# Kernel optimization log

Hardware: AMD Instinct MI355X
Metric: run time of the kernel (lower is better)

## Reference

```python
import jax, jax.numpy as jnp
import numpy as np

N_NODES = 50000


def _add_self_loops(edge_index, n):
    loop = jnp.arange(n, dtype=edge_index.dtype)
    src = jnp.concatenate([edge_index[0], loop])
    dst = jnp.concatenate([edge_index[1], loop])
    return src, dst


def _gcn_norm(src, dst, n):
    # symmetric normalization with unit edge weights (edge_weight=None)
    w = jnp.ones(src.shape[0], dtype=jnp.float32)
    deg = jax.ops.segment_sum(w, dst, num_segments=n)  # [N]
    dinv = jnp.where(deg > 0, jax.lax.rsqrt(jnp.maximum(deg, 1.0)), 0.0)
    return dinv[src] * w * dinv[dst]  # [E+N]


def _gcn_conv(x, src, dst, norm, W, b, n):
    h = x @ W                                   # [N, out] transform first (PyG order)
    msg = h[src] * norm[:, None]                # [E+N, out] gather + scale
    agg = jax.ops.segment_sum(msg, dst, num_segments=n)  # scatter-add
    return agg + b


def setup_inputs() -> dict:
    key = jax.random.key(0)
    k1, k2, k3, k4 = jax.random.split(key, 4)
    N, E, IN, HID, OUT = N_NODES, 1600000, 512, 64, 7
    x = jax.random.normal(k1, (N, IN), dtype=jnp.float32)
    edge_index = jax.random.randint(k2, (2, E), 0, N, dtype=jnp.int64)
    W1 = jax.random.normal(k3, (IN, HID), dtype=jnp.float32) * (1.0 / np.sqrt(IN))
    b1 = jnp.zeros((HID,), dtype=jnp.float32)
    W2 = jax.random.normal(k4, (HID, OUT), dtype=jnp.float32) * (1.0 / np.sqrt(HID))
    b2 = jnp.zeros((OUT,), dtype=jnp.float32)
    return {"x": x, "edge_index": edge_index, "W1": W1, "b1": b1, "W2": W2, "b2": b2}


def reference(x, edge_index, W1, b1, W2, b2):
    n = x.shape[0]
    src, dst = _add_self_loops(edge_index, n)
    norm = _gcn_norm(src, dst, n)  # graph-only, shared across layers
    h = _gcn_conv(x, src, dst, norm, W1, b1, n)
    h = jax.nn.relu(h)
    # dropout is identity in eval/inference mode
    out = _gcn_conv(h, src, dst, norm, W2, b2, n)
    return out
```

## Files before the change

kernel.cpp:

```cpp
#include <hip/hip_runtime.h>

#define N_NODES 50000
#define N_EDGES 1600000
#define DIM_IN  512
#define DIM_HID 64
#define DIM_OUT 7
#define NBUCK   196
#define PART_BLOCKS 256

using u16 = unsigned short;
using bf16x8 = __attribute__((ext_vector_type(8))) __bf16;
using f32x4  = __attribute__((ext_vector_type(4))) float;

__device__ __forceinline__ float bf2f(u16 u) {
    union { float f; unsigned int i; } v;
    v.i = ((unsigned int)u) << 16;
    return v.f;
}

__device__ __forceinline__ u16 f2bf(float f) {
    union { float f; unsigned int i; } v;
    v.f = f;
    unsigned int r = 0x7FFFu + ((v.i >> 16) & 1u);
    return (u16)((v.i + r) >> 16);
}

__global__ void k_detect(const u16* __restrict__ xw, const int* __restrict__ ei32,
                         int* __restrict__ flags) {
    __shared__ int s1[256];
    __shared__ int s2[256];
    int t = threadIdx.x;
    u16 w = xw[2 * t];
    int e = (w >> 7) & 0xFF;
    s1[t] = (e >= 100 && e <= 140) ? 1 : 0;
    s2[t] = (ei32[2 * t + 1] != 0) ? 1 : 0;
    __syncthreads();
    for (int off = 128; off >= 1; off >>= 1) {
        if (t < off) { s1[t] += s1[t + off]; s2[t] += s2[t + off]; }
        __syncthreads();
    }
    if (t == 0) {
        flags[0] = (s1[0] >= 200) ? 0 : 1;
        flags[1] = (s2[0] == 0) ? 1 : 0;
    }
}

__device__ __forceinline__ int ld_edge(const int* ei, int i64f, size_t idx) {
    if (i64f) return ei[2 * idx];
    return ei[idx];
}

__global__ void k_count(const int* __restrict__ ei, const int* __restrict__ flags,
                        int* __restrict__ gbsum, int* __restrict__ cnt) {
    __shared__ int hist[NBUCK];
    int t = threadIdx.x;
    int i64f = flags[1];
    const int CH = (N_EDGES + PART_BLOCKS - 1) / PART_BLOCKS;
    int lo = blockIdx.x * CH;
    int hi = lo + CH; if (hi > N_EDGES) hi = N_EDGES;
    if (t < NBUCK) hist[t] = 0;
    __syncthreads();
    for (int i = lo + t; i < hi; i += 1024) {
        int s = ld_edge(ei, i64f, (size_t)i);
        int d = ld_edge(ei, i64f, (size_t)N_EDGES + i);
        if ((unsigned)d < (unsigned)N_NODES && (unsigned)s < (unsigned)N_NODES)
            atomicAdd(&hist[d >> 8], 1);
    }
    __syncthreads();
    if (t < NBUCK) {
        int h = hist[t];
        cnt[t * PART_BLOCKS + blockIdx.x] = h;
        if (h > 0) atomicAdd(&gbsum[t], h);
    }
}

__global__ void k_pb(const int* __restrict__ gbsum, int* __restrict__ cnt,
                     int* __restrict__ bbase, int* __restrict__ rowptr) {
    __shared__ int g0[256];
    __shared__ int gs[256];
    __shared__ int sc[256];
    int b = blockIdx.x, t = threadIdx.x;
    int gv = (t < NBUCK) ? gbsum[t] : 0;
    g0[t] = gv;
    gs[t] = gv;
    __syncthreads();
    for (int off = 1; off < 256; off <<= 1) {
        int u = (t >= off) ? gs[t - off] : 0;
        __syncthreads();
        gs[t] += u;
        __syncthreads();
    }
    int bb = gs[b] - g0[b];
    if (t == 0) bbase[b] = bb;
    if (b == 0 && t == 255) rowptr[N_NODES] = gs[255];
    int v = cnt[b * PART_BLOCKS + t];
    sc[t] = v;
    __syncthreads();
    for (int off = 1; off < 256; off <<= 1) {
        int u = (t >= off) ? sc[t - off] : 0;
        __syncthreads();
        sc[t] += u;
        __syncthreads();
    }
    cnt[b * PART_BLOCKS + t] = bb + sc[t] - v;
}

__global__ void k_part(const int* __restrict__ ei, const int* __restrict__ flags,
                       const int* __restrict__ cnt, unsigned int* __restrict__ ebuf) {
    __shared__ int cur[NBUCK];
    int t = threadIdx.x, blk = blockIdx.x;
    int i64f = flags[1];
    const int CH = (N_EDGES + PART_BLOCKS - 1) / PART_BLOCKS;
    int lo = blk * CH;
    int hi = lo + CH; if (hi > N_EDGES) hi = N_EDGES;
    if (t < NBUCK) cur[t] = cnt[t * PART_BLOCKS + blk];
    __syncthreads();
    for (int i = lo + t; i < hi; i += 1024) {
        int s = ld_edge(ei, i64f, (size_t)i);
        int d = ld_edge(ei, i64f, (size_t)N_EDGES + i);
        if ((unsigned)d < (unsigned)N_NODES && (unsigned)s < (unsigned)N_NODES) {
            int pos = atomicAdd(&cur[d >> 8], 1);
            if ((unsigned)pos < (unsigned)N_EDGES)
                ebuf[pos] = ((unsigned)s << 8) | (unsigned)(d & 255);
        }
    }
}

__global__ void k_cfill(const unsigned int* __restrict__ ebuf,
                        const int* __restrict__ bbase, const int* __restrict__ gbsum,
                        int* __restrict__ rowptr, float* __restrict__ dinv,
                        int* __restrict__ col) {
    __shared__ int dcnt[256];
    __shared__ int sc[256];
    __shared__ int cur[256];
    int b = blockIdx.x, t = threadIdx.x;
    int e0 = bbase[b];
    int e1 = e0 + gbsum[b];
    if (t < 256) dcnt[t] = 0;
    __syncthreads();
    for (int e = e0 + t; e < e1; e += 1024)
        atomicAdd(&dcnt[ebuf[e] & 255u], 1);
    __syncthreads();
    int v = 0;
    if (t < 256) { v = dcnt[t]; sc[t] = v; }
    __syncthreads();
    for (int off = 1; off < 256; off <<= 1) {
        int u = (t >= off && t < 256) ? sc[t - off] : 0;
        __syncthreads();
        if (t < 256) sc[t] += u;
        __syncthreads();
    }
    if (t < 256) {
        int row0 = e0 + sc[t] - v;
        cur[t] = row0;
        int idx = b * 256 + t;
        if (idx < N_NODES) {
            rowptr[idx] = row0;
            dinv[idx] = rsqrtf((float)(v + 1));
        }
    }
    __syncthreads();
    for (int e = e0 + t; e < e1; e += 1024) {
        unsigned int x = ebuf[e];
        int p = atomicAdd(&cur[x & 255u], 1);
        if ((unsigned)p < (unsigned)N_EDGES) col[p] = (int)(x >> 8);
    }
}

__global__ void k_tw1(const void* __restrict__ W1, const int* __restrict__ flags,
                      u16* __restrict__ W1T) {
    int i = blockIdx.x * blockDim.x + threadIdx.x;
    if (i < DIM_IN * DIM_HID) {
        int n = i >> 9;
        int k = i & 511;
        if (flags[0]) W1T[i] = f2bf(((const float*)W1)[k * DIM_HID + n]);
        else          W1T[i] = ((const u16*)W1)[k * DIM_HID + n];
    }
}

__launch_bounds__(256)
__global__ void k_gemm1(const void* __restrict__ xraw, const u16* __restrict__ W1T,
                        const int* __restrict__ flags, const float* __restrict__ dinv,
                        u16* __restrict__ hs) {
    int f32f = flags[0];
    int wave = threadIdx.x >> 6;
    int lane = threadIdx.x & 63;
    int m16 = lane & 15;
    int quad = lane >> 4;
    int rbase = blockIdx.x * 64 + wave * 16;
    int ra = rbase + m16;
    if (ra > N_NODES - 1) ra = N_NODES - 1;
    const u16*   xrow_b = (const u16*)xraw   + (size_t)ra * DIM_IN + quad * 8;
    const float* xrow_f = (const float*)xraw + (size_t)ra * DIM_IN + quad * 8;
    const u16* wrow = W1T + (size_t)m16 * DIM_IN + quad * 8;

    f32x4 acc0 = {0.f, 0.f, 0.f, 0.f};
    f32x4 acc1 = {0.f, 0.f, 0.f, 0.f};
    f32x4 acc2 = {0.f, 0.f, 0.f, 0.f};
    f32x4 acc3 = {0.f, 0.f, 0.f, 0.f};

    for (int ks = 0; ks < DIM_IN / 32; ++ks) {
        bf16x8 a;
        if (f32f) {
            const float4* q = reinterpret_cast<const float4*>(xrow_f + ks * 32);
            float4 p0 = q[0], p1 = q[1];
            union { bf16x8 v; u16 s[8]; } u;
            u.s[0] = f2bf(p0.x); u.s[1] = f2bf(p0.y); u.s[2] = f2bf(p0.z); u.s[3] = f2bf(p0.w);
            u.s[4] = f2bf(p1.x); u.s[5] = f2bf(p1.y); u.s[6] = f2bf(p1.z); u.s[7] = f2bf(p1.w);
            a = u.v;
        } else {
            a = *reinterpret_cast<const bf16x8*>(xrow_b + ks * 32);
        }
        bf16x8 b0 = *reinterpret_cast<const bf16x8*>(wrow + ks * 32);
        bf16x8 b1 = *reinterpret_cast<const bf16x8*>(wrow + ks * 32 + 16 * DIM_IN);
        bf16x8 b2 = *reinterpret_cast<const bf16x8*>(wrow + ks * 32 + 32 * DIM_IN);
        bf16x8 b3 = *reinterpret_cast<const bf16x8*>(wrow + ks * 32 + 48 * DIM_IN);
        acc0 = __builtin_amdgcn_mfma_f32_16x16x32_bf16(a, b0, acc0, 0, 0, 0);
        acc1 = __builtin_amdgcn_mfma_f32_16x16x32_bf16(a, b1, acc1, 0, 0, 0);
        acc2 = __builtin_amdgcn_mfma_f32_16x16x32_bf16(a, b2, acc2, 0, 0, 0);
        acc3 = __builtin_amdgcn_mfma_f32_16x16x32_bf16(a, b3, acc3, 0, 0, 0);
    }

#pragma unroll
    for (int i = 0; i < 4; ++i) {
        int r = rbase + quad * 4 + i;
        if (r < N_NODES) {
            float dv = dinv[r];
            u16* orow = hs + (size_t)r * DIM_HID;
            orow[ 0 + m16] = f2bf(acc0[i] * dv);
            orow[16 + m16] = f2bf(acc1[i] * dv);
            orow[32 + m16] = f2bf(acc2[i] * dv);
            orow[48 + m16] = f2bf(acc3[i] * dv);
        }
    }
}

__launch_bounds__(256)
__global__ void k_agg1(const u16* __restrict__ hs, const int* __restrict__ rowptr,
                       const int* __restrict__ col, const float* __restrict__ dinv,
                       const void* __restrict__ b1, const void* __restrict__ W2,
                       const int* __restrict__ flags, float* __restrict__ zs) {
    int f32f = flags[0];
    int wave = threadIdx.x >> 6;
    int lane = threadIdx.x & 63;
    int d = blockIdx.x * 4 + wave;
    if (d >= N_NODES) return;
    int start = rowptr[d], end = rowptr[d + 1];
    if (start < 0) start = 0;
    if (end > N_EDGES) end = N_EDGES;
    if (end < start) end = start;

    float acc = bf2f(hs[(size_t)d * DIM_HID + lane]);

    for (int base = start; base < end; base += 64) {
        int rem = end - base; if (rem > 64) rem = 64;
        int ce = base + lane;
        int c = (ce < end) ? col[ce] : 0;
        for (int j0 = 0; j0 < rem; j0 += 16) {
            float v[16];
#pragma unroll
            for (int j = 0; j < 16; ++j) {
                int cj = __shfl(c, j0 + j);
                v[j] = (j0 + j < rem) ? bf2f(hs[(size_t)cj * DIM_HID + lane]) : 0.f;
            }
#pragma unroll
            for (int j = 0; j < 16; ++j) acc += v[j];
        }
    }

    float b1v = f32f ? ((const float*)b1)[lane] : bf2f(((const u16*)b1)[lane]);
    float dv = dinv[d];
    float h2 = fmaxf(acc * dv + b1v, 0.f);

    float p[7];
#pragma unroll
    for (int f = 0; f < 7; ++f) {
        float w = f32f ? ((const float*)W2)[lane * DIM_OUT + f]
                       : bf2f(((const u16*)W2)[lane * DIM_OUT + f]);
        p[f] = h2 * w;
    }
#pragma unroll
    for (int off = 32; off >= 1; off >>= 1) {
#pragma unroll
        for (int f = 0; f < 7; ++f) p[f] += __shfl_xor(p[f], off);
    }
    if (lane == 0) {
#pragma unroll
        for (int f = 0; f < 7; ++f) zs[(size_t)d * 8 + f] = p[f] * dv;
        zs[(size_t)d * 8 + 7] = 0.f;
    }
}

__launch_bounds__(256)
__global__ void k_agg2(const float* __restrict__ zs, const int* __restrict__ rowptr,
                       const int* __restrict__ col, const float* __restrict__ dinv,
                       const void* __restrict__ b2, const int* __restrict__ flags,
                       float* __restrict__ out) {
    int f32f = flags[0];
    int wave = threadIdx.x >> 6;
    int lane = threadIdx.x & 63;
    int d = blockIdx.x * 4 + wave;
    if (d >= N_NODES) return;
    int f = lane & 7;
    int g = lane >> 3;
    int start = rowptr[d], end = rowptr[d + 1];
    if (start < 0) start = 0;
    if (end > N_EDGES) end = N_EDGES;
    if (end < start) end = start;

    float acc = 0.f;
    for (int e = start + g; e < end; e += 8)
        acc += zs[(size_t)col[e] * 8 + f];

    acc += __shfl_xor(acc, 8);
    acc += __shfl_xor(acc, 16);
    acc += __shfl_xor(acc, 32);

    if (lane < 7) {
        float b2v = f32f ? ((const float*)b2)[lane] : bf2f(((const u16*)b2)[lane]);
        float tot = (acc + zs[(size_t)d * 8 + lane]) * dinv[d] + b2v;
        out[(size_t)d * DIM_OUT + lane] = tot;
    }
}

extern "C" void kernel_launch(void* const* d_in, const int* in_sizes, int n_in,
                              void* d_out, int out_size, void* d_ws, size_t ws_size,
                              hipStream_t stream) {
    const void* x  = d_in[0];
    const int*  ei = (const int*)d_in[1];
    const void* W1 = d_in[2];
    const void* b1 = d_in[3];
    const void* W2 = d_in[4];
    const void* b2 = d_in[5];

    char* ws = (char*)d_ws;
    size_t off = 0;
    auto alloc = [&](size_t bytes) -> void* {
        void* p = ws + off;
        off = (off + bytes + 255) & ~(size_t)255;
        return p;
    };
    int*   flags  = (int*)alloc(32);
    int*   rowptr = (int*)alloc((size_t)(N_NODES + 1) * 4);
    int*   gbsum  = (int*)alloc((size_t)NBUCK * 4);
    int*   bbase  = (int*)alloc((size_t)NBUCK * 4);
    int*   cnt    = (int*)alloc((size_t)NBUCK * PART_BLOCKS * 4);
    float* dinv   = (float*)alloc((size_t)N_NODES * 4);
    u16*   W1T    = (u16*)alloc((size_t)DIM_IN * DIM_HID * 2);
    unsigned int* ebuf = (unsigned int*)alloc((size_t)N_EDGES * 4);
    int*   colb   = (int*)alloc((size_t)N_EDGES * 4);
    u16*   hs     = (u16*)alloc((size_t)N_NODES * DIM_HID * 2);
    float* zs     = (float*)alloc((size_t)N_NODES * 8 * 4);
    float* out    = (float*)d_out;

    hipMemsetAsync(gbsum, 0, (size_t)NBUCK * 4, stream);
    k_detect<<<1, 256, 0, stream>>>((const u16*)x, ei, flags);
    k_count<<<PART_BLOCKS, 1024, 0, stream>>>(ei, flags, gbsum, cnt);
    k_pb   <<<NBUCK, 256, 0, stream>>>(gbsum, cnt, bbase, rowptr);
    k_part <<<PART_BLOCKS, 1024, 0, stream>>>(ei, flags, cnt, ebuf);
    k_cfill<<<NBUCK, 1024, 0, stream>>>(ebuf, bbase, gbsum, rowptr, dinv, colb);
    k_tw1  <<<(DIM_IN * DIM_HID + 255) / 256, 256, 0, stream>>>(W1, flags, W1T);
    k_gemm1<<<(N_NODES + 63) / 64, 256, 0, stream>>>(x, W1T, flags, dinv, hs);
    k_agg1 <<<(N_NODES + 3) / 4, 256, 0, stream>>>(hs, rowptr, colb, dinv, b1, W2, flags, zs);
    k_agg2 <<<(N_NODES + 3) / 4, 256, 0, stream>>>(zs, rowptr, colb, dinv, b2, flags, out);
}
```

Baseline: 341.7 us.

## Vectorize layer-1 aggregation with 16-byte row-slice loads across 8 edge groups

Restructures the first-layer aggregation so each wave processes 8 edges at once, with every 8-lane group loading one neighbor's 128-byte bf16 row as uint4 slices. The loop is unrolled by four edges per group for more memory-level parallelism, and partial sums are combined with xor shuffles. A shared-memory transpose then redistributes the per-feature results for the W2 projection. This replaces per-lane 2-byte gathers with wide loads and fewer shuffle-broadcasts of column indices. The early return for out-of-range nodes was removed because the kernel now calls __syncthreads, so it relies on the node count dividing evenly by four.

After: 296.1 us. -13.4%, faster.

```diff
diff --git a/kernel.cpp b/kernel.cpp
--- a/kernel.cpp
+++ b/kernel.cpp
@@ -23,6 +23,18 @@
     v.f = f;
     unsigned int r = 0x7FFFu + ((v.i >> 16) & 1u);
     return (u16)((v.i + r) >> 16);
+}
+
+__device__ __forceinline__ float bflo(unsigned int u) {
+    union { float f; unsigned int i; } v;
+    v.i = u << 16;
+    return v.f;
+}
+
+__device__ __forceinline__ float bfhi(unsigned int u) {
+    union { float f; unsigned int i; } v;
+    v.i = u & 0xFFFF0000u;
+    return v.f;
 }
 
 __global__ void k_detect(const u16* __restrict__ xw, const int* __restrict__ ei32,
@@ -240,37 +252,99 @@
                        const int* __restrict__ col, const float* __restrict__ dinv,
                        const void* __restrict__ b1, const void* __restrict__ W2,
                        const int* __restrict__ flags, float* __restrict__ zs) {
+    __shared__ float xh[4][64];
     int f32f = flags[0];
     int wave = threadIdx.x >> 6;
     int lane = threadIdx.x & 63;
+    int g = lane >> 3;
+    int q = lane & 7;
     int d = blockIdx.x * 4 + wave;
-    if (d >= N_NODES) return;
     int start = rowptr[d], end = rowptr[d + 1];
     if (start < 0) start = 0;
     if (end > N_EDGES) end = N_EDGES;
     if (end < start) end = start;
 
-    float acc = bf2f(hs[(size_t)d * DIM_HID + lane]);
-
-    for (int base = start; base < end; base += 64) {
-        int rem = end - base; if (rem > 64) rem = 64;
-        int ce = base + lane;
-        int c = (ce < end) ? col[ce] : 0;
-        for (int j0 = 0; j0 < rem; j0 += 16) {
-            float v[16];
-#pragma unroll
-            for (int j = 0; j < 16; ++j) {
-                int cj = __shfl(c, j0 + j);
-                v[j] = (j0 + j < rem) ? bf2f(hs[(size_t)cj * DIM_HID + lane]) : 0.f;
-            }
-#pragma unroll
-            for (int j = 0; j < 16; ++j) acc += v[j];
-        }
-    }
-
-    float b1v = f32f ? ((const float*)b1)[lane] : bf2f(((const u16*)b1)[lane]);
+    float a[8];
+#pragma unroll
+    for (int k = 0; k < 8; ++k) a[k] = 0.f;
+
+    const uint4* hs4 = reinterpret_cast<const uint4*>(hs);
+    const int* cp = col + start;
+    int ne = end - start;
+    int nfull = ne >> 3;
+
+    int it = 0;
+    for (; it + 4 <= nfull; it += 4) {
+        int c0 = cp[(it + 0) * 8 + g];
+        int c1 = cp[(it + 1) * 8 + g];
+        int c2 = cp[(it + 2) * 8 + g];
+        int c3 = cp[(it + 3) * 8 + g];
+        uint4 r0 = hs4[(size_t)c0 * 8 + q];
+        uint4 r1 = hs4[(size_t)c1 * 8 + q];
+        uint4 r2 = hs4[(size_t)c2 * 8 + q];
+        uint4 r3 = hs4[(size_t)c3 * 8 + q];
+#pragma unroll
+        for (int u = 0; u < 4; ++u) {
+            uint4 r = (u == 0) ? r0 : (u == 1) ? r1 : (u == 2) ? r2 : r3;
+            a[0] += bflo(r.x); a[1] += bfhi(r.x);
+            a[2] += bflo(r.y); a[3] += bfhi(r.y);
+            a[4] += bflo(r.z); a[5] += bfhi(r.z);
+            a[6] += bflo(r.w); a[7] += bfhi(r.w);
+        }
+    }
+    for (; it < nfull; ++it) {
+        int c = cp[it * 8 + g];
+        uint4 r = hs4[(size_t)c * 8 + q];
+        a[0] += bflo(r.x); a[1] += bfhi(r.x);
+        a[2] += bflo(r.y); a[3] += bfhi(r.y);
+        a[4] += bflo(r.z); a[5] += bfhi(r.z);
+        a[6] += bflo(r.w); a[7] += bfhi(r.w);
+    }
+    {
+        int e = start + nfull * 8 + g;
+        if (e < end) {
+            int c = col[e];
+            uint4 r = hs4[(size_t)c * 8 + q];
+            a[0] += bflo(r.x); a[1] += bfhi(r.x);
+            a[2] += bflo(r.y); a[3] += bfhi(r.y);
+            a[4] += bflo(r.z); a[5] += bfhi(r.z);
+            a[6] += bflo(r.w); a[7] += bfhi(r.w);
+        }
+    }
+
+#pragma unroll
+    for (int k = 0; k < 8; ++k) {
+        a[k] += __shfl_xor(a[k], 8);
+        a[k] += __shfl_xor(a[k], 16);
+        a[k] += __shfl_xor(a[k], 32);
+    }
+
+    {
+        uint4 r = hs4[(size_t)d * 8 + q];
+        a[0] += bflo(r.x); a[1] += bfhi(r.x);
+        a[2] += bflo(r.y); a[3] += bfhi(r.y);
+        a[4] += bflo(r.z); a[5] += bfhi(r.z);
+        a[6] += bflo(r.w); a[7] += bfhi(r.w);
+    }
+
     float dv = dinv[d];
-    float h2 = fmaxf(acc * dv + b1v, 0.f);
+    float h[8];
+    if (f32f) {
+        const float* bf = (const float*)b1 + q * 8;
+#pragma unroll
+        for (int k = 0; k < 8; ++k) h[k] = fmaxf(a[k] * dv + bf[k], 0.f);
+    } else {
+        const u16* bb = (const u16*)b1 + q * 8;
+#pragma unroll
+        for (int k = 0; k < 8; ++k) h[k] = fmaxf(a[k] * dv + bf2f(bb[k]), 0.f);
+    }
+
+    if (g == 0) {
+#pragma unroll
+        for (int k = 0; k < 8; ++k) xh[wave][q * 8 + k] = h[k];
+    }
+    __syncthreads();
+    float h2 = xh[wave][lane];
 
     float p[7];
 #pragma unroll
```
